# Optimization experiments

Measured on AMD Instinct MI355X. Metric: run time of the kernel, lower is better.

Reference implementation:

```python
import jax, jax.numpy as jnp
import numpy as np

B, N, E = 8, 5000, 80000
NODE_IN, EDGE_IN, HIDDEN, EMBED = 32, 16, 128, 64


def setup_inputs() -> dict:
    key = jax.random.key(0)
    ks = jax.random.split(key, 20)
    g = lambda k, shape: jax.random.normal(k, shape, dtype=jnp.float32) * 0.05
    return {
        "node_x": jax.random.normal(ks[0], (B, N, NODE_IN), dtype=jnp.float32),
        "edge_attr": jax.random.normal(ks[1], (B, E, EDGE_IN), dtype=jnp.float32),
        "edge_index": jax.random.randint(ks[2], (2, E), 0, N),
        "ln_node_g": jnp.ones((NODE_IN,), jnp.float32),
        "ln_node_b": jnp.zeros((NODE_IN,), jnp.float32),
        "ln_edge_g": jnp.ones((EDGE_IN,), jnp.float32),
        "ln_edge_b": jnp.zeros((EDGE_IN,), jnp.float32),
        "gat0_W": g(ks[3], (NODE_IN, HIDDEN)),
        "gat0_We": g(ks[4], (EDGE_IN, HIDDEN)),
        "gat0_asrc": g(ks[5], (HIDDEN,)),
        "gat0_adst": g(ks[6], (HIDDEN,)),
        "gat0_ae": g(ks[7], (HIDDEN,)),
        "gat0_b": jnp.zeros((HIDDEN,), jnp.float32),
        "gat1_W": g(ks[8], (HIDDEN, EMBED)),
        "gat1_We": g(ks[9], (EDGE_IN, EMBED)),
        "gat1_asrc": g(ks[10], (EMBED,)),
        "gat1_adst": g(ks[11], (EMBED,)),
        "gat1_ae": g(ks[12], (EMBED,)),
        "gat1_b": jnp.zeros((EMBED,), jnp.float32),
        "mlp_W1": g(ks[13], (4 * EMBED + EDGE_IN, HIDDEN)),
        "mlp_b1": jnp.zeros((HIDDEN,), jnp.float32),
        "mlp_W2": g(ks[14], (HIDDEN, 1)),
        "mlp_b2": jnp.zeros((1,), jnp.float32),
    }


def _layernorm(x, g, b, eps=1e-5):
    mu = x.mean(-1, keepdims=True)
    var = ((x - mu) ** 2).mean(-1, keepdims=True)
    return (x - mu) * jax.lax.rsqrt(var + eps) * g + b


def _gat_layer(x, efeat, src, dst, W, We, asrc, adst, ae, b, nseg):
    # Single-head GATConv with edge features: attention logits from src/dst/edge projections,
    # segment-softmax over incoming edges per destination node, weighted-sum aggregation.
    h = x @ W                      # [nseg, out]
    he = efeat @ We                # [num_edges, out]
    logits = jax.nn.leaky_relu(
        (h[src] * asrc).sum(-1) + (h[dst] * adst).sum(-1) + (he * ae).sum(-1), 0.2)
    m = jax.ops.segment_max(logits, dst, num_segments=nseg)
    m = jnp.where(jnp.isfinite(m), m, 0.0)
    ex = jnp.exp(logits - m[dst])
    denom = jax.ops.segment_sum(ex, dst, num_segments=nseg)
    alpha = ex / (denom[dst] + 1e-16)
    return jax.ops.segment_sum(alpha[:, None] * h[src], dst, num_segments=nseg) + b


def reference(node_x, edge_attr, edge_index, ln_node_g, ln_node_b, ln_edge_g, ln_edge_b,
              gat0_W, gat0_We, gat0_asrc, gat0_adst, gat0_ae, gat0_b,
              gat1_W, gat1_We, gat1_asrc, gat1_adst, gat1_ae, gat1_b,
              mlp_W1, mlp_b1, mlp_W2, mlp_b2):
    nx = _layernorm(node_x, ln_node_g, ln_node_b)
    ea = _layernorm(edge_attr, ln_edge_g, ln_edge_b)
    # Batched graph: offset shared edge_index per graph.
    xf = nx.reshape(B * N, NODE_IN)
    ef = ea.reshape(B * E, EDGE_IN)
    offs = jnp.arange(B) * N
    ei = (edge_index[:, None, :] + offs[None, :, None]).reshape(2, B * E)
    src, dst = ei[0], ei[1]
    batch_vec = jnp.repeat(jnp.arange(B), N)
    # GAT encoder: layer 0 (ELU) then final projection to embed.
    h = jax.nn.elu(_gat_layer(xf, ef, src, dst, gat0_W, gat0_We, gat0_asrc, gat0_adst, gat0_ae, gat0_b, B * N))
    node_emb = _gat_layer(h, ef, src, dst, gat1_W, gat1_We, gat1_asrc, gat1_adst, gat1_ae, gat1_b, B * N)
    # Global context: concat(mean, max) pooling per graph -> [B, 2*EMBED]
    mean_pool = jax.ops.segment_sum(node_emb, batch_vec, num_segments=B) / N
    max_pool = jax.ops.segment_max(node_emb, batch_vec, num_segments=B)
    ctx = jnp.concatenate([mean_pool, max_pool], axis=-1)
    # Per-edge gather-concat + MLP
    edge_emb = jnp.concatenate([node_emb[src], node_emb[dst], ef, ctx[batch_vec[src]]], axis=-1)
    hm = jax.nn.relu(edge_emb @ mlp_W1 + mlp_b1)
    q = (hm @ mlp_W2 + mlp_b2).squeeze(-1)
    return q.reshape(B, E)
```

## Files before the change

### kernel.cpp

```cpp
#include <hip/hip_runtime.h>
#include <cmath>

#define BB 8
#define NN 5000
#define EE 80000
#define NODE_IN 32
#define EDGE_IN 16
#define HIDDEN 128
#define EMBED 64
#define BN (BB*NN)
#define BE (BB*EE)

typedef unsigned short u16;
typedef __attribute__((ext_vector_type(8))) __bf16 bf16x8;
typedef __attribute__((ext_vector_type(4))) float f32x4;

__device__ __forceinline__ float waveSum(float v){
  #pragma unroll
  for(int o=32;o;o>>=1) v += __shfl_xor(v,o);
  return v;
}
__device__ __forceinline__ float waveMax(float v){
  #pragma unroll
  for(int o=32;o;o>>=1) v = fmaxf(v,__shfl_xor(v,o));
  return v;
}
__device__ __forceinline__ int rlanei(int v, int l){
  return __builtin_amdgcn_readlane(v, l);
}
__device__ __forceinline__ float rlanef(float v, int l){
  return __uint_as_float(__builtin_amdgcn_readlane(__float_as_uint(v), l));
}
__device__ __forceinline__ unsigned pack_bf2(float a0, float a1){
  unsigned u0 = __float_as_uint(a0), u1 = __float_as_uint(a1);
  unsigned r0 = (u0 + 0x7fffu + ((u0>>16)&1u)) >> 16;
  unsigned r1 = (u1 + 0x7fffu + ((u1>>16)&1u)) & 0xffff0000u;
  return r0 | r1;
}
__device__ __forceinline__ u16 bf16r(float x){
  unsigned u = __float_as_uint(x);
  return (u16)((u + 0x7fffu + ((u>>16)&1u)) >> 16);
}
__device__ __forceinline__ float bflo(unsigned h){ return __uint_as_float(h<<16); }
__device__ __forceinline__ float bfhi(unsigned h){ return __uint_as_float(h & 0xffff0000u); }

__launch_bounds__(256)
__global__ void k_prep(const float* We0, const float* ae0,
                       const float* We1, const float* ae1,
                       const float* W1g, const float* asrc1, const float* adst1,
                       const float* mlpW1,
                       float* wae, float* ws1, float* wd1,
                       u16* BT1u, u16* BT2u){
  int t = threadIdx.x;
  if(blockIdx.x == 0){
    if(t < 16){
      float a = 0.f;
      for(int k=0;k<HIDDEN;k++) a += We0[t*HIDDEN+k]*ae0[k];
      wae[t] = a;
    } else if(t < 32){
      int j = t-16;
      float a = 0.f;
      for(int k=0;k<EMBED;k++) a += We1[j*EMBED+k]*ae1[k];
      wae[16+j] = a;
    }
    if(t < 128){
      float s = 0.f, d = 0.f;
      for(int k=0;k<EMBED;k++){
        float w = W1g[t*EMBED+k];
        s += w*asrc1[k];
        d += w*adst1[k];
      }
      ws1[t] = s; wd1[t] = d;
    }
  } else {
    #pragma unroll
    for(int ii=0; ii<6; ii++){
      int idx = (blockIdx.x-1)*1536 + ii*256 + t;
      if(idx < 8192){
        int c = idx >> 7, k = idx & 127;
        BT1u[c*136 + k] = bf16r(W1g[k*EMBED + c]);
      } else {
        int i2 = idx - 8192;
        int d = i2 >> 6, j = i2 & 63;
        float v = (d < 128) ? mlpW1[j*HIDDEN + d] : mlpW1[(64+j)*HIDDEN + (d-128)];
        BT2u[d*72 + j] = bf16r(v);
      }
    }
  }
}

__launch_bounds__(256)
__global__ void k_node(const float* __restrict__ x, const float* __restrict__ g,
                       const float* __restrict__ bb, const float* __restrict__ W,
                       const float* __restrict__ asrc, const float* __restrict__ adst,
                       unsigned* __restrict__ H0u, float* __restrict__ S0o, float* __restrict__ D0o){
  int t = threadIdx.x;
  int w = t>>6, lane = t&63;
  float w0r[NODE_IN], w1r[NODE_IN];
  #pragma unroll
  for(int j=0;j<NODE_IN;j++){
    w0r[j] = W[j*HIDDEN + 2*lane];
    w1r[j] = W[j*HIDDEN + 2*lane + 1];
  }
  float gl = (lane<NODE_IN)? g[lane] : 0.f;
  float bl = (lane<NODE_IN)? bb[lane] : 0.f;
  float asl0 = asrc[2*lane], asl1 = asrc[2*lane+1];
  float adl0 = adst[2*lane], adl1 = adst[2*lane+1];
  for(int nb = blockIdx.x; nb < BN/4; nb += gridDim.x){
    int n = nb*4 + w;
    float xv = (lane<NODE_IN)? x[n*NODE_IN+lane] : 0.f;
    float s  = waveSum(xv);
    float s2 = waveSum(xv*xv);
    float mu = s*(1.f/NODE_IN);
    float var = s2*(1.f/NODE_IN) - mu*mu;
    float inv = 1.0f / sqrtf(var + 1e-5f);
    float nx = (lane<NODE_IN)? ((xv-mu)*inv*gl + bl) : 0.f;
    float a0=0.f, a1=0.f;
    #pragma unroll
    for(int j=0;j<NODE_IN;j++){
      float r = rlanef(nx, j);
      a0 += r*w0r[j];
      a1 += r*w1r[j];
    }
    H0u[(size_t)n*64 + lane] = pack_bf2(a0, a1);
    float sv = waveSum(a0*asl0 + a1*asl1);
    float dv = waveSum(a0*adl0 + a1*adl1);
    if(lane==0){ S0o[n]=sv; D0o[n]=dv; }
  }
}

__launch_bounds__(256)
__global__ void k_edge(const float* __restrict__ ein, const float* __restrict__ g,
                       const float* __restrict__ bb, const float* __restrict__ wae,
                       const int* __restrict__ EPOS,
                       float* __restrict__ EAp, float* __restrict__ E0p, float* __restrict__ E1p){
  int ge = blockIdx.x*256 + threadIdx.x;
  int b = ge / EE, e = ge - b*EE;
  int gp = b*EE + EPOS[e];
  float v[EDGE_IN];
  const float4* p = (const float4*)(ein + (size_t)ge*EDGE_IN);
  float4 q0=p[0], q1=p[1], q2=p[2], q3=p[3];
  v[0]=q0.x; v[1]=q0.y; v[2]=q0.z; v[3]=q0.w;
  v[4]=q1.x; v[5]=q1.y; v[6]=q1.z; v[7]=q1.w;
  v[8]=q2.x; v[9]=q2.y; v[10]=q2.z; v[11]=q2.w;
  v[12]=q3.x; v[13]=q3.y; v[14]=q3.z; v[15]=q3.w;
  float s=0.f, s2=0.f;
  #pragma unroll
  for(int j=0;j<EDGE_IN;j++){ s += v[j]; s2 += v[j]*v[j]; }
  float mu = s*(1.f/EDGE_IN);
  float var = s2*(1.f/EDGE_IN) - mu*mu;
  float inv = 1.0f / sqrtf(var + 1e-5f);
  float e0=0.f, e1=0.f;
  #pragma unroll
  for(int j=0;j<EDGE_IN;j++){
    float nv = (v[j]-mu)*inv*g[j] + bb[j];
    v[j] = nv;
    e0 += nv*wae[j];
    e1 += nv*wae[16+j];
  }
  float4* q = (float4*)(EAp + (size_t)gp*EDGE_IN);
  q[0] = make_float4(v[0],v[1],v[2],v[3]);
  q[1] = make_float4(v[4],v[5],v[6],v[7]);
  q[2] = make_float4(v[8],v[9],v[10],v[11]);
  q[3] = make_float4(v[12],v[13],v[14],v[15]);
  E0p[gp]=e0; E1p[gp]=e1;
}

__global__ void k_count(const int* __restrict__ ei, int* __restrict__ cnt){
  int e = blockIdx.x*256 + threadIdx.x;
  if(e < EE) atomicAdd(&cnt[ei[EE+e]], 1);
}

__launch_bounds__(1024)
__global__ void k_scan(int* __restrict__ off, int* __restrict__ cur){
  __shared__ int part[1024];
  int t = threadIdx.x;
  int loc[5]; int s=0;
  int base = t*5;
  #pragma unroll
  for(int k=0;k<5;k++){ int idx=base+k; int c=(idx<NN)? cur[idx]:0; loc[k]=s; s+=c; }
  part[t]=s;
  __syncthreads();
  for(int o=1;o<1024;o<<=1){
    int v = (t>=o)? part[t-o] : 0;
    __syncthreads();
    part[t] += v;
    __syncthreads();
  }
  int pre = (t>0)? part[t-1] : 0;
  #pragma unroll
  for(int k=0;k<5;k++){
    int idx=base+k;
    if(idx<NN){ int o2 = pre+loc[k]; off[idx]=o2; cur[idx]=o2; }
  }
  if(t==0) off[NN] = EE;
}

__global__ void k_fill(const int* __restrict__ ei, int* __restrict__ cur,
                       int* __restrict__ csrc, int* __restrict__ cdst,
                       int* __restrict__ ceid, int* __restrict__ epos){
  int e = blockIdx.x*256 + threadIdx.x;
  if(e < EE){
    int d = ei[EE+e];
    int pos = atomicAdd(&cur[d], 1);
    csrc[pos] = ei[e];
    cdst[pos] = d;
    ceid[pos] = e;
    epos[e] = pos;
  }
}

__launch_bounds__(256)
__global__ void k_gat0(const unsigned* __restrict__ H0u, const float* __restrict__ S0,
                       const float* __restrict__ D0, const float* __restrict__ E0p,
                       const int* __restrict__ off, const int* __restrict__ csrc,
                       const float* __restrict__ bias,
                       const float* __restrict__ WS1, const float* __restrict__ WD1,
                       unsigned* __restrict__ HELUu, float* __restrict__ S1o, float* __restrict__ D1o){
  int t = threadIdx.x, w = t>>6, lane = t&63;
  int b = blockIdx.x & 7, c = blockIdx.x >> 3;
  int n = c*4 + w;
  int gid = b*NN + n;
  int base = off[n], deg = off[n+1]-base;
  const float* s0b = S0 + b*NN;
  const float* e0b = E0p + b*EE;
  const unsigned* h0b = H0u + (size_t)b*NN*64;
  float dv = D0[gid];
  float acc0=0.f, acc1=0.f;
  if(deg > 0){
    if(deg <= 64){
      float lg = -INFINITY; int sidx = 0;
      if(lane < deg){
        sidx = csrc[base+lane];
        float xx = s0b[sidx] + dv + e0b[base+lane];
        lg = xx>0.f ? xx : 0.2f*xx;
      }
      float m = waveMax(lg);
      float ex = (lane<deg)? __expf(lg-m) : 0.f;
      float den = waveSum(ex);
      float al = ex / (den + 1e-16f);
      int nb8 = (deg+7)>>3;
      for(int b8=0;b8<nb8;b8++){
        int i0 = b8*8;
        int ss[8]; float aa[8]; unsigned hh[8];
        #pragma unroll
        for(int kk=0;kk<8;kk++){ ss[kk]=rlanei(sidx, i0+kk); aa[kk]=rlanef(al, i0+kk); }
        #pragma unroll
        for(int kk=0;kk<8;kk++){ hh[kk]=h0b[ss[kk]*64 + lane]; }
        #pragma unroll
        for(int kk=0;kk<8;kk++){ acc0 += aa[kk]*bflo(hh[kk]); acc1 += aa[kk]*bfhi(hh[kk]); }
      }
    } else {
      float m = -INFINITY;
      for(int i=lane;i<deg;i+=64){
        float xx = s0b[csrc[base+i]] + dv + e0b[base+i];
        xx = xx>0.f ? xx : 0.2f*xx;
        m = fmaxf(m, xx);
      }
      m = waveMax(m);
      float den = 0.f;
      for(int i=lane;i<deg;i+=64){
        float xx = s0b[csrc[base+i]] + dv + e0b[base+i];
        xx = xx>0.f ? xx : 0.2f*xx;
        den += __expf(xx-m);
      }
      den = waveSum(den) + 1e-16f;
      for(int i=0;i<deg;i++){
        int s = csrc[base+i];
        float xx = s0b[s] + dv + e0b[base+i];
        xx = xx>0.f ? xx : 0.2f*xx;
        float a = __expf(xx-m)/den;
        unsigned h = h0b[s*64 + lane];
        acc0 += a*bflo(h);
        acc1 += a*bfhi(h);
      }
    }
  }
  float2 bi = *(const float2*)&bias[2*lane];
  float v0 = acc0 + bi.x;
  float v1 = acc1 + bi.y;
  v0 = v0>0.f ? v0 : (__expf(v0)-1.f);
  v1 = v1>0.f ? v1 : (__expf(v1)-1.f);
  HELUu[(size_t)gid*64 + lane] = pack_bf2(v0, v1);
  float2 wsv = *(const float2*)&WS1[2*lane];
  float2 wdv = *(const float2*)&WD1[2*lane];
  float sv1 = waveSum(v0*wsv.x + v1*wsv.y);
  float dv1 = waveSum(v0*wdv.x + v1*wdv.y);
  if(lane==0){ S1o[gid]=sv1; D1o[gid]=dv1; }
}

__launch_bounds__(256)
__global__ void k_h1(const unsigned* __restrict__ HELUu, const u16* __restrict__ BT1,
                     u16* __restrict__ H1u){
  __shared__ u16 Ald[64*136];
  __shared__ u16 Bld[64*136];
  int t = threadIdx.x;
  int n0 = blockIdx.x*64;
  #pragma unroll
  for(int ii=0; ii<4; ii++){
    int c2 = ii*256 + t;
    int r = c2 >> 4, q = c2 & 15;
    *(uint4*)&Ald[r*136 + q*8] = ((const uint4*)(HELUu + (size_t)(n0+r)*64))[q];
  }
  for(int i=t; i<1088; i+=256) ((uint4*)Bld)[i] = ((const uint4*)BT1)[i];
  __syncthreads();
  int w = t>>6, lane = t&63;
  int lo = lane & 15, hi = lane >> 4;
  f32x4 acc0 = {0.f,0.f,0.f,0.f}, acc1 = acc0, acc2 = acc0, acc3 = acc0;
  #pragma unroll
  for(int ks=0; ks<4; ks++){
    bf16x8 a = *(const bf16x8*)&Ald[(w*16+lo)*136 + ks*32 + hi*8];
    bf16x8 b0 = *(const bf16x8*)&Bld[(0*16+lo)*136 + ks*32 + hi*8];
    bf16x8 b1 = *(const bf16x8*)&Bld[(1*16+lo)*136 + ks*32 + hi*8];
    bf16x8 b2 = *(const bf16x8*)&Bld[(2*16+lo)*136 + ks*32 + hi*8];
    bf16x8 b3 = *(const bf16x8*)&Bld[(3*16+lo)*136 + ks*32 + hi*8];
    acc0 = __builtin_amdgcn_mfma_f32_16x16x32_bf16(a, b0, acc0, 0,0,0);
    acc1 = __builtin_amdgcn_mfma_f32_16x16x32_bf16(a, b1, acc1, 0,0,0);
    acc2 = __builtin_amdgcn_mfma_f32_16x16x32_bf16(a, b2, acc2, 0,0,0);
    acc3 = __builtin_amdgcn_mfma_f32_16x16x32_bf16(a, b3, acc3, 0,0,0);
  }
  int rowb = n0 + w*16 + hi*4;
  #pragma unroll
  for(int r=0;r<4;r++){
    H1u[(size_t)(rowb+r)*64 +  0 + lo] = bf16r(acc0[r]);
    H1u[(size_t)(rowb+r)*64 + 16 + lo] = bf16r(acc1[r]);
    H1u[(size_t)(rowb+r)*64 + 32 + lo] = bf16r(acc2[r]);
    H1u[(size_t)(rowb+r)*64 + 48 + lo] = bf16r(acc3[r]);
  }
}

__launch_bounds__(256)
__global__ void k_gat1(const u16* __restrict__ H1u, const float* __restrict__ S1,
                       const float* __restrict__ D1, const float* __restrict__ E1p,
                       const int* __restrict__ off, const int* __restrict__ csrc,
                       const float* __restrict__ bias, float* __restrict__ out){
  int t = threadIdx.x, w = t>>6, lane = t&63;
  int b = blockIdx.x & 7, c = blockIdx.x >> 3;
  int n = c*4 + w;
  int gid = b*NN + n;
  int base = off[n], deg = off[n+1]-base;
  const float* s1b = S1 + b*NN;
  const float* e1b = E1p + b*EE;
  const u16* h1b = H1u + (size_t)b*NN*64;
  float dv = D1[gid];
  float acc = 0.f;
  if(deg > 0){
    if(deg <= 64){
      float lg = -INFINITY; int sidx = 0;
      if(lane < deg){
        sidx = csrc[base+lane];
        float xx = s1b[sidx] + dv + e1b[base+lane];
        lg = xx>0.f ? xx : 0.2f*xx;
      }
      float m = waveMax(lg);
      float ex = (lane<deg)? __expf(lg-m) : 0.f;
      float den = waveSum(ex);
      float al = ex / (den + 1e-16f);
      int nb8 = (deg+7)>>3;
      for(int b8=0;b8<nb8;b8++){
        int i0 = b8*8;
        int ss[8]; float aa[8]; unsigned hh[8];
        #pragma unroll
        for(int kk=0;kk<8;kk++){ ss[kk]=rlanei(sidx, i0+kk); aa[kk]=rlanef(al, i0+kk); }
        #pragma unroll
        for(int kk=0;kk<8;kk++){ hh[kk]=h1b[ss[kk]*64 + lane]; }
        #pragma unroll
        for(int kk=0;kk<8;kk++){ acc += aa[kk]*__uint_as_float(hh[kk]<<16); }
      }
    } else {
      float m = -INFINITY;
      for(int i=lane;i<deg;i+=64){
        float xx = s1b[csrc[base+i]] + dv + e1b[base+i];
        xx = xx>0.f ? xx : 0.2f*xx;
        m = fmaxf(m, xx);
      }
      m = waveMax(m);
      float den = 0.f;
      for(int i=lane;i<deg;i+=64){
        float xx = s1b[csrc[base+i]] + dv + e1b[base+i];
        xx = xx>0.f ? xx : 0.2f*xx;
        den += __expf(xx-m);
      }
      den = waveSum(den) + 1e-16f;
      for(int i=0;i<deg;i++){
        int s = csrc[base+i];
        float xx = s1b[s] + dv + e1b[base+i];
        xx = xx>0.f ? xx : 0.2f*xx;
        float a = __expf(xx-m)/den;
        acc += a*__uint_as_float(((unsigned)h1b[s*64 + lane])<<16);
      }
    }
  }
  out[(size_t)gid*EMBED + lane] = acc + bias[lane];
}

__launch_bounds__(256)
__global__ void k_pool(const float* __restrict__ EMBp, float* __restrict__ PSUM,
                       float* __restrict__ PMAX){
  int blk = blockIdx.x & 31, b = blockIdx.x >> 5;
  int t = threadIdx.x;
  int dim = t & 63, chunk = t >> 6;
  int n0 = blk*157, n1 = n0+157 < NN ? n0+157 : NN;
  float sm = 0.f, mx = -INFINITY;
  for(int n=n0+chunk; n<n1; n+=4){
    float v = EMBp[((size_t)(b*NN+n))*EMBED + dim];
    sm += v; mx = fmaxf(mx, v);
  }
  __shared__ float ssum[256], smax[256];
  ssum[t]=sm; smax[t]=mx;
  __syncthreads();
  if(t < 64){
    float S = ssum[t]+ssum[t+64]+ssum[t+128]+ssum[t+192];
    float M = fmaxf(fmaxf(smax[t],smax[t+64]), fmaxf(smax[t+128],smax[t+192]));
    PSUM[(b*32+blk)*64 + t] = S;
    PMAX[(b*32+blk)*64 + t] = M;
  }
}

__launch_bounds__(128)
__global__ void k_ctxp(const float* __restrict__ PSUM, const float* __restrict__ PMAX,
                       const float* __restrict__ W1, const float* __restrict__ b1,
                       float* __restrict__ CTXP){
  int b = blockIdx.x, c = threadIdx.x;
  __shared__ float cl[128];
  if(c < 64){
    float S = 0.f;
    for(int k=0;k<32;k++) S += PSUM[(b*32+k)*64 + c];
    cl[c] = S*(1.f/NN);
  } else {
    float M = -INFINITY;
    for(int k=0;k<32;k++) M = fmaxf(M, PMAX[(b*32+k)*64 + (c-64)]);
    cl[c] = M;
  }
  __syncthreads();
  float a = b1[c];
  for(int j=0;j<128;j++) a += cl[j]*W1[(144+j)*HIDDEN + c];
  CTXP[b*128+c] = a;
}

__launch_bounds__(256)
__global__ void k_psd(const float* __restrict__ EMB, const u16* __restrict__ BT2,
                      u16* __restrict__ PSu, u16* __restrict__ PDu){
  __shared__ u16 Ald[64*72];
  __shared__ u16 Bld[256*72];
  int t = threadIdx.x;
  int n0 = blockIdx.x*64;
  #pragma unroll
  for(int ii=0; ii<2; ii++){
    int c2 = ii*256 + t;
    int r = c2 >> 3, q = c2 & 7;
    const float4* src = (const float4*)(EMB + (size_t)(n0+r)*EMBED + q*8);
    float4 f0 = src[0], f1 = src[1];
    uint4 pk = make_uint4(pack_bf2(f0.x,f0.y), pack_bf2(f0.z,f0.w),
                          pack_bf2(f1.x,f1.y), pack_bf2(f1.z,f1.w));
    *(uint4*)&Ald[r*72 + q*8] = pk;
  }
  for(int i=t; i<2304; i+=256) ((uint4*)Bld)[i] = ((const uint4*)BT2)[i];
  __syncthreads();
  int w = t>>6, lane = t&63;
  int lo = lane & 15, hi = lane >> 4;
  f32x4 acc[16];
  #pragma unroll
  for(int i=0;i<16;i++) acc[i] = (f32x4){0.f,0.f,0.f,0.f};
  #pragma unroll
  for(int ks=0; ks<2; ks++){
    bf16x8 a = *(const bf16x8*)&Ald[(w*16+lo)*72 + ks*32 + hi*8];
    #pragma unroll
    for(int nt=0; nt<16; nt++){
      bf16x8 b = *(const bf16x8*)&Bld[(nt*16+lo)*72 + ks*32 + hi*8];
      acc[nt] = __builtin_amdgcn_mfma_f32_16x16x32_bf16(a, b, acc[nt], 0,0,0);
    }
  }
  int rowb = n0 + w*16 + hi*4;
  #pragma unroll
  for(int nt=0; nt<16; nt++){
    #pragma unroll
    for(int r=0;r<4;r++){
      u16 u = bf16r(acc[nt][r]);
      if(nt < 8) PSu[(size_t)(rowb+r)*HIDDEN + nt*16 + lo] = u;
      else       PDu[(size_t)(rowb+r)*HIDDEN + (nt-8)*16 + lo] = u;
    }
  }
}

__launch_bounds__(256)
__global__ void k_final(const float* __restrict__ EAp, const int* __restrict__ csrc,
                        const int* __restrict__ cdst, const int* __restrict__ ceid,
                        const unsigned* __restrict__ PS, const unsigned* __restrict__ PD,
                        const float* __restrict__ CTXP, const float* __restrict__ W1,
                        const float* __restrict__ W2, const float* __restrict__ b2,
                        float* __restrict__ out){
  int t = threadIdx.x, w = t>>6, lane = t&63;
  int b = blockIdx.x & 7, c = blockIdx.x >> 3;
  int p0 = c*128 + w*32;
  float w1r0[16], w1r1[16];
  #pragma unroll
  for(int j=0;j<16;j++){
    float2 wv = *(const float2*)&W1[(128+j)*HIDDEN + 2*lane];
    w1r0[j]=wv.x; w1r1[j]=wv.y;
  }
  float2 w2v = *(const float2*)&W2[2*lane];
  float2 cpv = *(const float2*)&CTXP[b*128 + 2*lane];
  float bias2 = b2[0];
  int sv=0, dvv=0, ev=0;
  if(lane<32){ sv=csrc[p0+lane]; dvv=cdst[p0+lane]; ev=ceid[p0+lane]; }
  const unsigned* PSb = PS + (size_t)b*NN*64;
  const unsigned* PDb = PD + (size_t)b*NN*64;
  const float4* EAsrc = (const float4*)(EAp + ((size_t)b*EE + p0)*EDGE_IN);
  float4 f0 = EAsrc[2*lane], f1 = EAsrc[2*lane+1];
  float fr[8] = {f0.x,f0.y,f0.z,f0.w, f1.x,f1.y,f1.z,f1.w};
  float myq = 0.f;
  #pragma unroll
  for(int g=0; g<8; g++){
    int i0 = g*4;
    int ss[4], dd[4];
    #pragma unroll
    for(int kk=0;kk<4;kk++){ ss[kk]=rlanei(sv, i0+kk); dd[kk]=rlanei(dvv, i0+kk); }
    unsigned ps[4], pd[4];
    #pragma unroll
    for(int kk=0;kk<4;kk++){ ps[kk]=PSb[ss[kk]*64 + lane]; }
    #pragma unroll
    for(int kk=0;kk<4;kk++){ pd[kk]=PDb[dd[kk]*64 + lane]; }
    float p[4];
    #pragma unroll
    for(int kk=0;kk<4;kk++){
      float h0 = cpv.x + bflo(ps[kk]) + bflo(pd[kk]);
      float h1 = cpv.y + bfhi(ps[kk]) + bfhi(pd[kk]);
      #pragma unroll
      for(int j=0;j<16;j++){
        int flat = (i0+kk)*16 + j;
        float aj = rlanef(fr[flat & 7], flat >> 3);
        h0 += aj*w1r0[j];
        h1 += aj*w1r1[j];
      }
      h0 = fmaxf(h0, 0.f);
      h1 = fmaxf(h1, 0.f);
      p[kk] = h0*w2v.x + h1*w2v.y;
    }
    #pragma unroll
    for(int kk=0;kk<4;kk++){
      p[kk] += __shfl_xor(p[kk], 32);
      p[kk] += __shfl_xor(p[kk], 16);
    }
    int q = lane>>4;
    float sel = (q==0)? p[0] : (q==1)? p[1] : (q==2)? p[2] : p[3];
    sel += __shfl_xor(sel, 8);
    sel += __shfl_xor(sel, 4);
    sel += __shfl_xor(sel, 2);
    sel += __shfl_xor(sel, 1);
    #pragma unroll
    for(int kk=0;kk<4;kk++){
      float tot = rlanef(sel, kk*16);
      if(lane == i0+kk) myq = tot;
    }
  }
  if(lane < 32) out[(size_t)b*EE + ev] = myq + bias2;
}

extern "C" void kernel_launch(void* const* d_in, const int* in_sizes, int n_in,
                              void* d_out, int out_size, void* d_ws, size_t ws_size,
                              hipStream_t stream) {
  const float* node_x   = (const float*)d_in[0];
  const float* edge_attr= (const float*)d_in[1];
  const int*   edge_idx = (const int*)d_in[2];
  const float* ln_ng    = (const float*)d_in[3];
  const float* ln_nb    = (const float*)d_in[4];
  const float* ln_eg    = (const float*)d_in[5];
  const float* ln_eb    = (const float*)d_in[6];
  const float* g0_W     = (const float*)d_in[7];
  const float* g0_We    = (const float*)d_in[8];
  const float* g0_asrc  = (const float*)d_in[9];
  const float* g0_adst  = (const float*)d_in[10];
  const float* g0_ae    = (const float*)d_in[11];
  const float* g0_b     = (const float*)d_in[12];
  const float* g1_W     = (const float*)d_in[13];
  const float* g1_We    = (const float*)d_in[14];
  const float* g1_asrc  = (const float*)d_in[15];
  const float* g1_adst  = (const float*)d_in[16];
  const float* g1_ae    = (const float*)d_in[17];
  const float* g1_b     = (const float*)d_in[18];
  const float* mlp_W1   = (const float*)d_in[19];
  const float* mlp_b1   = (const float*)d_in[20];
  const float* mlp_W2   = (const float*)d_in[21];
  const float* mlp_b2   = (const float*)d_in[22];
  float* out = (float*)d_out;

  float* ws   = (float*)d_ws;
  float* EAp  = ws;
  float* E0p  = EAp  + (size_t)BE*EDGE_IN;
  float* E1p  = E0p  + BE;
  float* H0   = E1p  + BE;
  float* HELU = H0   + (size_t)BN*HIDDEN;
  float* H1   = HELU + (size_t)BN*HIDDEN;
  float* EMBa = H1   + (size_t)BN*EMBED;
  float* S0   = EMBa + (size_t)BN*EMBED;
  float* D0   = S0 + BN;
  float* S1   = D0 + BN;
  float* D1   = S1 + BN;
  float* CTX  = D1 + BN;
  float* CTXP = CTX + 1024;
  float* WAE  = CTXP + 1024;
  int* CSR_OFF = (int*)(WAE + 32);
  int* CSR_CUR = CSR_OFF + (NN+4);
  int* CSR_SRC = CSR_CUR + NN;
  int* CSR_DST = CSR_SRC + EE;
  int* CSR_EID = CSR_DST + EE;
  int* EPOS    = CSR_EID + EE;
  float* WS1   = (float*)(EPOS + EE);
  float* WD1   = WS1 + 128;
  u16* BT1u    = (u16*)(WD1 + 128);
  u16* BT2u    = BT1u + 64*136;
  float* PSUM  = (float*)(BT2u + 256*72);
  float* PMAX  = PSUM + 256*64;
  unsigned* H0u   = (unsigned*)H0;
  unsigned* HELUu = (unsigned*)HELU;
  u16*      H1u   = (u16*)H1;
  unsigned* PS = (unsigned*)H0;
  unsigned* PD = (unsigned*)HELU;

  hipMemsetAsync(CSR_CUR, 0, NN*sizeof(int), stream);
  k_prep<<<17, 256, 0, stream>>>(g0_We, g0_ae, g1_We, g1_ae, g1_W, g1_asrc, g1_adst,
                                 mlp_W1, WAE, WS1, WD1, BT1u, BT2u);
  k_count<<<(EE+255)/256, 256, 0, stream>>>(edge_idx, CSR_CUR);
  k_scan<<<1, 1024, 0, stream>>>(CSR_OFF, CSR_CUR);
  k_fill<<<(EE+255)/256, 256, 0, stream>>>(edge_idx, CSR_CUR, CSR_SRC, CSR_DST, CSR_EID, EPOS);
  k_node<<<1024, 256, 0, stream>>>(node_x, ln_ng, ln_nb, g0_W, g0_asrc, g0_adst, H0u, S0, D0);
  k_edge<<<BE/256, 256, 0, stream>>>(edge_attr, ln_eg, ln_eb, WAE, EPOS, EAp, E0p, E1p);
  k_gat0<<<BN/4, 256, 0, stream>>>(H0u, S0, D0, E0p, CSR_OFF, CSR_SRC, g0_b, WS1, WD1, HELUu, S1, D1);
  k_h1<<<BN/64, 256, 0, stream>>>(HELUu, BT1u, H1u);
  k_gat1<<<BN/4, 256, 0, stream>>>(H1u, S1, D1, E1p, CSR_OFF, CSR_SRC, g1_b, EMBa);
  k_pool<<<256, 256, 0, stream>>>(EMBa, PSUM, PMAX);
  k_ctxp<<<BB, 128, 0, stream>>>(PSUM, PMAX, mlp_W1, mlp_b1, CTXP);
  k_psd<<<BN/64, 256, 0, stream>>>(EMBa, BT2u, (u16*)PS, (u16*)PD);
  k_final<<<BE/128, 256, 0, stream>>>(EAp, CSR_SRC, CSR_DST, CSR_EID, PS, PD, CTXP, mlp_W1, mlp_W2, mlp_b2, out);
}
```

Before: 362.4 us.

## Compute final edge MLP with MFMA and fold context into node projections

The per-edge final MLP, which did scalar FMAs with readlane broadcasts, now computes the edge-feature part of the first layer with bf16 MFMA. Its output is laid out so each lane adds gathered bf16 source/destination projections and reduces against W2 with a few shuffles. Edge features are stored as bf16 instead of fp32, which halves that traffic. The per-graph context term is folded, half each, into the PS/PD node projections in k_psd, so k_final no longer loads it. This adds bf16 rounding of the edge features and of the context-folded projections, and wastes half the MFMA K dimension on zero padding.

```diff
diff --git a/kernel.cpp b/kernel.cpp
--- a/kernel.cpp
+++ b/kernel.cpp
@@ -43,6 +43,10 @@
 }
 __device__ __forceinline__ float bflo(unsigned h){ return __uint_as_float(h<<16); }
 __device__ __forceinline__ float bfhi(unsigned h){ return __uint_as_float(h & 0xffff0000u); }
+__device__ __forceinline__ bf16x8 ld8_or_zero(const u16* p, bool pred){
+  uint4 v = pred ? *(const uint4*)p : make_uint4(0u,0u,0u,0u);
+  return *(bf16x8*)&v;
+}
 
 __launch_bounds__(256)
 __global__ void k_prep(const float* We0, const float* ae0,
@@ -50,7 +54,7 @@
                        const float* W1g, const float* asrc1, const float* adst1,
                        const float* mlpW1,
                        float* wae, float* ws1, float* wd1,
-                       u16* BT1u, u16* BT2u){
+                       u16* BT1u, u16* BT2u, u16* AT1e){
   int t = threadIdx.x;
   if(blockIdx.x == 0){
     if(t < 16){
@@ -71,6 +75,10 @@
         d += w*adst1[k];
       }
       ws1[t] = s; wd1[t] = d;
+    }
+    for(int i=t; i<2048; i+=256){
+      int o = i >> 4, k = i & 15;
+      AT1e[o*16 + k] = bf16r(mlpW1[(128+k)*HIDDEN + o]);
     }
   } else {
     #pragma unroll
@@ -133,7 +141,7 @@
 __global__ void k_edge(const float* __restrict__ ein, const float* __restrict__ g,
                        const float* __restrict__ bb, const float* __restrict__ wae,
                        const int* __restrict__ EPOS,
-                       float* __restrict__ EAp, float* __restrict__ E0p, float* __restrict__ E1p){
+                       u16* __restrict__ EAb, float* __restrict__ E0p, float* __restrict__ E1p){
   int ge = blockIdx.x*256 + threadIdx.x;
   int b = ge / EE, e = ge - b*EE;
   int gp = b*EE + EPOS[e];
@@ -158,11 +166,12 @@
     e0 += nv*wae[j];
     e1 += nv*wae[16+j];
   }
-  float4* q = (float4*)(EAp + (size_t)gp*EDGE_IN);
-  q[0] = make_float4(v[0],v[1],v[2],v[3]);
-  q[1] = make_float4(v[4],v[5],v[6],v[7]);
-  q[2] = make_float4(v[8],v[9],v[10],v[11]);
-  q[3] = make_float4(v[12],v[13],v[14],v[15]);
+  uint4 w0 = make_uint4(pack_bf2(v[0],v[1]), pack_bf2(v[2],v[3]),
+                        pack_bf2(v[4],v[5]), pack_bf2(v[6],v[7]));
+  uint4 w1 = make_uint4(pack_bf2(v[8],v[9]), pack_bf2(v[10],v[11]),
+                        pack_bf2(v[12],v[13]), pack_bf2(v[14],v[15]));
+  uint4* q = (uint4*)&EAb[(size_t)gp*16];
+  q[0] = w0; q[1] = w1;
   E0p[gp]=e0; E1p[gp]=e1;
 }
 
@@ -440,6 +449,7 @@
 
 __launch_bounds__(256)
 __global__ void k_psd(const float* __restrict__ EMB, const u16* __restrict__ BT2,
+                      const float* __restrict__ CTXP,
                       u16* __restrict__ PSu, u16* __restrict__ PDu){
   __shared__ u16 Ald[64*72];
   __shared__ u16 Bld[256*72];
@@ -473,88 +483,76 @@
   }
   int rowb = n0 + w*16 + hi*4;
   #pragma unroll
-  for(int nt=0; nt<16; nt++){
-    #pragma unroll
-    for(int r=0;r<4;r++){
-      u16 u = bf16r(acc[nt][r]);
-      if(nt < 8) PSu[(size_t)(rowb+r)*HIDDEN + nt*16 + lo] = u;
-      else       PDu[(size_t)(rowb+r)*HIDDEN + (nt-8)*16 + lo] = u;
-    }
-  }
-}
-
-__launch_bounds__(256)
-__global__ void k_final(const float* __restrict__ EAp, const int* __restrict__ csrc,
+  for(int r=0;r<4;r++){
+    int row = rowb + r;
+    int bg = row / NN;
+    const float* cp = CTXP + bg*128;
+    #pragma unroll
+    for(int nt=0; nt<16; nt++){
+      int dim = (nt & 7)*16 + lo;
+      u16 u = bf16r(acc[nt][r] + 0.5f*cp[dim]);
+      if(nt < 8) PSu[(size_t)row*HIDDEN + dim] = u;
+      else       PDu[(size_t)row*HIDDEN + dim] = u;
+    }
+  }
+}
+
+__launch_bounds__(256)
+__global__ void k_final(const u16* __restrict__ EAb, const int* __restrict__ csrc,
                         const int* __restrict__ cdst, const int* __restrict__ ceid,
-                        const unsigned* __restrict__ PS, const unsigned* __restrict__ PD,
-                        const float* __restrict__ CTXP, const float* __restrict__ W1,
+                        const u16* __restrict__ PS, const u16* __restrict__ PD,
+                        const u16* __restrict__ AT1e,
                         const float* __restrict__ W2, const float* __restrict__ b2,
                         float* __restrict__ out){
   int t = threadIdx.x, w = t>>6, lane = t&63;
+  int lo = lane & 15, hi = lane >> 4;
   int b = blockIdx.x & 7, c = blockIdx.x >> 3;
   int p0 = c*128 + w*32;
-  float w1r0[16], w1r1[16];
-  #pragma unroll
-  for(int j=0;j<16;j++){
-    float2 wv = *(const float2*)&W1[(128+j)*HIDDEN + 2*lane];
-    w1r0[j]=wv.x; w1r1[j]=wv.y;
-  }
-  float2 w2v = *(const float2*)&W2[2*lane];
-  float2 cpv = *(const float2*)&CTXP[b*128 + 2*lane];
+  bf16x8 afr[8];
+  #pragma unroll
+  for(int mt=0;mt<8;mt++) afr[mt] = ld8_or_zero(&AT1e[(mt*16+lo)*16 + hi*8], hi<2);
+  float4 w2r[8];
+  #pragma unroll
+  for(int mt=0;mt<8;mt++) w2r[mt] = *(const float4*)&W2[mt*16 + hi*4];
   float bias2 = b2[0];
-  int sv=0, dvv=0, ev=0;
-  if(lane<32){ sv=csrc[p0+lane]; dvv=cdst[p0+lane]; ev=ceid[p0+lane]; }
-  const unsigned* PSb = PS + (size_t)b*NN*64;
-  const unsigned* PDb = PD + (size_t)b*NN*64;
-  const float4* EAsrc = (const float4*)(EAp + ((size_t)b*EE + p0)*EDGE_IN);
-  float4 f0 = EAsrc[2*lane], f1 = EAsrc[2*lane+1];
-  float fr[8] = {f0.x,f0.y,f0.z,f0.w, f1.x,f1.y,f1.z,f1.w};
-  float myq = 0.f;
-  #pragma unroll
-  for(int g=0; g<8; g++){
-    int i0 = g*4;
-    int ss[4], dd[4];
-    #pragma unroll
-    for(int kk=0;kk<4;kk++){ ss[kk]=rlanei(sv, i0+kk); dd[kk]=rlanei(dvv, i0+kk); }
-    unsigned ps[4], pd[4];
-    #pragma unroll
-    for(int kk=0;kk<4;kk++){ ps[kk]=PSb[ss[kk]*64 + lane]; }
-    #pragma unroll
-    for(int kk=0;kk<4;kk++){ pd[kk]=PDb[dd[kk]*64 + lane]; }
-    float p[4];
-    #pragma unroll
-    for(int kk=0;kk<4;kk++){
-      float h0 = cpv.x + bflo(ps[kk]) + bflo(pd[kk]);
-      float h1 = cpv.y + bfhi(ps[kk]) + bfhi(pd[kk]);
-      #pragma unroll
-      for(int j=0;j<16;j++){
-        int flat = (i0+kk)*16 + j;
-        float aj = rlanef(fr[flat & 7], flat >> 3);
-        h0 += aj*w1r0[j];
-        h1 += aj*w1r1[j];
-      }
-      h0 = fmaxf(h0, 0.f);
-      h1 = fmaxf(h1, 0.f);
-      p[kk] = h0*w2v.x + h1*w2v.y;
-    }
-    #pragma unroll
-    for(int kk=0;kk<4;kk++){
-      p[kk] += __shfl_xor(p[kk], 32);
-      p[kk] += __shfl_xor(p[kk], 16);
-    }
-    int q = lane>>4;
-    float sel = (q==0)? p[0] : (q==1)? p[1] : (q==2)? p[2] : p[3];
-    sel += __shfl_xor(sel, 8);
-    sel += __shfl_xor(sel, 4);
-    sel += __shfl_xor(sel, 2);
-    sel += __shfl_xor(sel, 1);
-    #pragma unroll
-    for(int kk=0;kk<4;kk++){
-      float tot = rlanef(sel, kk*16);
-      if(lane == i0+kk) myq = tot;
-    }
-  }
-  if(lane < 32) out[(size_t)b*EE + ev] = myq + bias2;
+  const u16* PSb = PS + (size_t)b*NN*HIDDEN;
+  const u16* PDb = PD + (size_t)b*NN*HIDDEN;
+  #pragma unroll
+  for(int g=0; g<2; g++){
+    int pg = p0 + g*16;
+    int s = csrc[pg + lo];
+    int d = cdst[pg + lo];
+    bf16x8 bfr = ld8_or_zero(&EAb[((size_t)b*EE + pg + lo)*16 + hi*8], hi<2);
+    const u16* pr = PSb + (size_t)s*HIDDEN + hi*4;
+    const u16* qr = PDb + (size_t)d*HIDDEN + hi*4;
+    uint2 psv[8], pdv[8];
+    #pragma unroll
+    for(int mt=0;mt<8;mt++) psv[mt] = *(const uint2*)(pr + mt*16);
+    #pragma unroll
+    for(int mt=0;mt<8;mt++) pdv[mt] = *(const uint2*)(qr + mt*16);
+    f32x4 acc[8];
+    #pragma unroll
+    for(int mt=0;mt<8;mt++){
+      f32x4 z = {0.f,0.f,0.f,0.f};
+      acc[mt] = __builtin_amdgcn_mfma_f32_16x16x32_bf16(afr[mt], bfr, z, 0,0,0);
+    }
+    float qp = 0.f;
+    #pragma unroll
+    for(int mt=0;mt<8;mt++){
+      float h0 = acc[mt][0] + bflo(psv[mt].x) + bflo(pdv[mt].x);
+      float h1 = acc[mt][1] + bfhi(psv[mt].x) + bfhi(pdv[mt].x);
+      float h2 = acc[mt][2] + bflo(psv[mt].y) + bflo(pdv[mt].y);
+      float h3 = acc[mt][3] + bfhi(psv[mt].y) + bfhi(pdv[mt].y);
+      qp += fmaxf(h0,0.f)*w2r[mt].x + fmaxf(h1,0.f)*w2r[mt].y
+          + fmaxf(h2,0.f)*w2r[mt].z + fmaxf(h3,0.f)*w2r[mt].w;
+    }
+    qp += __shfl_xor(qp, 16);
+    qp += __shfl_xor(qp, 32);
+    if(lane < 16){
+      int ev = ceid[pg + lane];
+      out[(size_t)b*EE + ev] = qp + bias2;
+    }
+  }
 }
 
 extern "C" void kernel_launch(void* const* d_in, const int* in_sizes, int n_in,
@@ -612,25 +610,27 @@
   u16* BT2u    = BT1u + 64*136;
   float* PSUM  = (float*)(BT2u + 256*72);
   float* PMAX  = PSUM + 256*64;
+  u16* AT1e    = (u16*)(PMAX + 256*64);
+  u16* EAb16      = (u16*)EAp;
   unsigned* H0u   = (unsigned*)H0;
   unsigned* HELUu = (unsigned*)HELU;
   u16*      H1u   = (u16*)H1;
-  unsigned* PS = (unsigned*)H0;
-  unsigned* PD = (unsigned*)HELU;
+  u16* PS = (u16*)H0;
+  u16* PD = (u16*)HELU;
 
   hipMemsetAsync(CSR_CUR, 0, NN*sizeof(int), stream);
   k_prep<<<17, 256, 0, stream>>>(g0_We, g0_ae, g1_We, g1_ae, g1_W, g1_asrc, g1_adst,
-                                 mlp_W1, WAE, WS1, WD1, BT1u, BT2u);
+                                 mlp_W1, WAE, WS1, WD1, BT1u, BT2u, AT1e);
   k_count<<<(EE+255)/256, 256, 0, stream>>>(edge_idx, CSR_CUR);
   k_scan<<<1, 1024, 0, stream>>>(CSR_OFF, CSR_CUR);
   k_fill<<<(EE+255)/256, 256, 0, stream>>>(edge_idx, CSR_CUR, CSR_SRC, CSR_DST, CSR_EID, EPOS);
   k_node<<<1024, 256, 0, stream>>>(node_x, ln_ng, ln_nb, g0_W, g0_asrc, g0_adst, H0u, S0, D0);
-  k_edge<<<BE/256, 256, 0, stream>>>(edge_attr, ln_eg, ln_eb, WAE, EPOS, EAp, E0p, E1p);
+  k_edge<<<BE/256, 256, 0, stream>>>(edge_attr, ln_eg, ln_eb, WAE, EPOS, EAb16, E0p, E1p);
   k_gat0<<<BN/4, 256, 0, stream>>>(H0u, S0, D0, E0p, CSR_OFF, CSR_SRC, g0_b, WS1, WD1, HELUu, S1, D1);
   k_h1<<<BN/64, 256, 0, stream>>>(HELUu, BT1u, H1u);
   k_gat1<<<BN/4, 256, 0, stream>>>(H1u, S1, D1, E1p, CSR_OFF, CSR_SRC, g1_b, EMBa);
   k_pool<<<256, 256, 0, stream>>>(EMBa, PSUM, PMAX);
   k_ctxp<<<BB, 128, 0, stream>>>(PSUM, PMAX, mlp_W1, mlp_b1, CTXP);
-  k_psd<<<BN/64, 256, 0, stream>>>(EMBa, BT2u, (u16*)PS, (u16*)PD);
-  k_final<<<BE/128, 256, 0, stream>>>(EAp, CSR_SRC, CSR_DST, CSR_EID, PS, PD, CTXP, mlp_W1, mlp_W2, mlp_b2, out);
-}
+  k_psd<<<BN/64, 256, 0, stream>>>(EMBa, BT2u, CTXP, PS, PD);
+  k_final<<<BE/128, 256, 0, stream>>>(EAb16, CSR_SRC, CSR_DST, CSR_EID, PS, PD, AT1e, mlp_W2, mlp_b2, out);
+}
```

New measurement: 336.1 us. 1.08x faster.
